# Optimization experiments

Hardware: AMD Instinct MI355X
Metric: run time of the kernel (lower is better)

The kernel has to match this reference:

```python
import jax, jax.numpy as jnp
import numpy as np

B, L, K, LI, D, NU, NI, C = 4096, 50, 10, 20, 64, 100000, 50000, 10


def _forward(users, items, u_items, u_items_mask, u_frids, u_frids_mask,
             u_frids_items, F_i, user_emb, item_emb, i_class,
             W1, b1, Wih, Whh, bih, bhh, W2, b2, W3, b3, W4, b4, W5, b5,
             W6, b6, alpha, lambdas):
    Bsz = users.shape[0]
    k = u_frids.shape[1]
    u = user_emb[users]                      # [B,d]
    i_e = item_emb[items]                    # [B,d]
    v = user_emb[u_frids]                    # [B,k,d]

    # ju_all = l1(cat(item_emb, i_class))
    ju_all = jnp.concatenate([item_emb, i_class], axis=1) @ W1 + b1   # [NI+1,d]
    ju = ju_all[u_items]                     # [B,L,d]

    # single-layer batch_first LSTM (torch gate order i,f,g,o)
    def step(carry, x):
        h, c = carry
        g = x @ Wih + h @ Whh + bih + bhh    # [B,4d]
        gi, gf, gg, go = jnp.split(g, 4, axis=1)
        c = jax.nn.sigmoid(gf) * c + jax.nn.sigmoid(gi) * jnp.tanh(gg)
        h = jax.nn.sigmoid(go) * jnp.tanh(c)
        return (h, c), h

    h0 = jnp.zeros((Bsz, ju.shape[-1]), ju.dtype)
    (_, _), hs = jax.lax.scan(step, (h0, h0), ju.transpose(1, 0, 2))
    out = hs.transpose(1, 0, 2)              # [B,L,d]
    hu = out[jnp.arange(Bsz), u_items_mask - 1]   # [B,d] last valid step

    hui = jnp.concatenate([hu, i_e, hu * i_e], axis=1) @ W2 + b2

    jv_all = jnp.concatenate([item_emb, i_class], axis=1) @ W3 + b3
    jv = jv_all[u_frids_items]               # [B,k,Li,d]
    # faithful to source: sum over item dim divided by friend count
    pv = jv.sum(axis=2) / u_frids_mask[:, None, None].astype(jv.dtype)  # [B,k,d]

    u_rep = jnp.broadcast_to(u[:, None, :], v.shape)
    at = jax.nn.leaky_relu(
        (jnp.concatenate([u_rep, v], axis=2) @ W4 + b4)[..., 0])  # [B,k]
    fmask = jnp.arange(k)[None, :] < u_frids_mask[:, None]
    auv = jnp.where(fmask,
                    jax.nn.softmax(jnp.where(fmask, at, -jnp.inf), axis=1),
                    0.0)                      # ragged softmax, zero-padded
    su = (pv * auv[:, :, None]).sum(axis=1)  # [B,d]
    sui = jnp.concatenate([su, i_e, su * i_e], axis=1) @ W5 + b5

    Fi1 = item_emb[F_i[:, 0, :]]             # [B,k,d]
    Fi2 = item_emb[F_i[:, 1, :]]
    i_rep = jnp.broadcast_to(i_e[:, None, :], Fi1.shape)
    s1 = jax.nn.leaky_relu(
        (jnp.concatenate([i_rep, Fi1], axis=2) @ W6 + b6)[..., 0])
    s2 = jax.nn.leaky_relu(
        (jnp.concatenate([i_rep, Fi2], axis=2) @ W6 + b6)[..., 0])
    # faithful to source: softmax over batch dim (dim=0)
    b1s = jax.nn.softmax(s1, axis=0)[:, :, None]
    b2s = jax.nn.softmax(s2, axis=0)[:, :, None]
    yi = alpha * (b1s * Fi1).sum(axis=1) + (1.0 - alpha) * (Fi2 * b2s).sum(axis=1)

    S = (lambdas[0] * (hu * yi).sum(1) + lambdas[1] * (hui * yi).sum(1)
         + lambdas[2] * (su * yi).sum(1) + lambdas[3] * (sui * yi).sum(1))
    return jax.nn.sigmoid(S)                 # rui [B]


def setup_inputs() -> dict:
    key = jax.random.key(0)
    ks = jax.random.split(key, 32)
    f32 = jnp.float32
    sd = 1.0 / np.sqrt(D)

    def lin(k, fan_in, fan_out):
        return sd * jax.random.normal(k, (fan_in, fan_out), dtype=f32)

    inp = {
        "users": jax.random.randint(ks[0], (B,), 0, NU),
        "items": jax.random.randint(ks[1], (B,), 0, NI),
        "u_items": jax.random.randint(ks[2], (B, L), 0, NI + 1),
        "u_items_mask": jax.random.randint(ks[3], (B,), 1, L + 1),
        "u_frids": jax.random.randint(ks[4], (B, K), 0, NU + 1),
        "u_frids_mask": jax.random.randint(ks[5], (B,), 1, K + 1),
        "u_frids_items": jax.random.randint(ks[6], (B, K, LI), 0, NI + 1),
        "F_i": jax.random.randint(ks[7], (B, 2, K), 0, NI + 1),
        "user_emb": sd * jax.random.normal(ks[8], (NU + 1, D), dtype=f32),
        "item_emb": sd * jax.random.normal(ks[9], (NI + 1, D), dtype=f32),
        "i_class": jax.nn.one_hot(
            jax.random.randint(ks[10], (NI + 1,), 0, C), C, dtype=f32),
        "W1": lin(ks[11], D + C, D), "b1": jnp.zeros((D,), f32),
        "Wih": lin(ks[12], D, 4 * D), "Whh": lin(ks[13], D, 4 * D),
        "bih": jnp.zeros((4 * D,), f32), "bhh": jnp.zeros((4 * D,), f32),
        "W2": lin(ks[14], 3 * D, D), "b2": jnp.zeros((D,), f32),
        "W3": lin(ks[15], D + C, D), "b3": jnp.zeros((D,), f32),
        "W4": lin(ks[16], 2 * D, 1), "b4": jnp.zeros((1,), f32),
        "W5": lin(ks[17], 3 * D, D), "b5": jnp.zeros((D,), f32),
        "W6": lin(ks[18], 2 * D, 1), "b6": jnp.zeros((1,), f32),
        "alpha": jnp.array([0.5], f32),
        "lambdas": jnp.array([0.5, 0.5, 0.5, 0.5], f32),
    }
    return inp


def reference(users, items, u_items, u_items_mask, u_frids, u_frids_mask,
              u_frids_items, F_i, user_emb, item_emb, i_class,
              W1, b1, Wih, Whh, bih, bhh, W2, b2, W3, b3, W4, b4, W5, b5,
              W6, b6, alpha, lambdas):
    return _forward(users, items, u_items, u_items_mask, u_frids,
                    u_frids_mask, u_frids_items, F_i, user_emb, item_emb,
                    i_class, W1, b1, Wih, Whh, bih, bhh, W2, b2, W3, b3,
                    W4, b4, W5, b5, W6, b6, alpha, lambdas)
```

## Files before the change

### kernel.cpp

```cpp
#include <hip/hip_runtime.h>

#define BSZ   4096
#define LSEQ  50
#define KFR   10
#define LI    20
#define DIM   64
#define NITEM 50001
#define CCLS  10

typedef __attribute__((ext_vector_type(8))) short short8;
typedef __attribute__((ext_vector_type(4))) float floatx4;

#define LOG2E 1.442695040888963f

__device__ inline unsigned short f2bf(float f) {
  unsigned u = __builtin_bit_cast(unsigned, f);
  u += 0x7FFF + ((u >> 16) & 1);
  return (unsigned short)(u >> 16);
}
__device__ inline float bf2f(unsigned short u) {
  return __builtin_bit_cast(float, ((unsigned)u) << 16);
}
__device__ inline float fast_exp(float x) {
  return __builtin_amdgcn_exp2f(x * LOG2E);
}
__device__ inline float fast_sigmoid(float x) {
  float e = __builtin_amdgcn_exp2f(-LOG2E * x);
  return __builtin_amdgcn_rcpf(1.0f + e);
}
__device__ inline float fast_tanh(float x) {
  float e = __builtin_amdgcn_exp2f(2.0f * LOG2E * x);
  return 1.0f - 2.0f * __builtin_amdgcn_rcpf(e + 1.0f);
}

__device__ __forceinline__ void item_block(int bid, int nblk,
                                 const float* __restrict__ item_emb,
                                 const float* __restrict__ i_class,
                                 const float* __restrict__ W1, const float* __restrict__ b1,
                                 const float* __restrict__ W3, const float* __restrict__ b3,
                                 unsigned short* __restrict__ ju_all,
                                 unsigned short* __restrict__ jv_all) {
  __shared__ float wcls[2][CCLS][64];
  for (int i = threadIdx.x; i < CCLS * 64; i += 256) {
    wcls[0][i >> 6][i & 63] = W1[(64 + (i >> 6)) * 64 + (i & 63)];
    wcls[1][i >> 6][i & 63] = W3[(64 + (i >> 6)) * 64 + (i & 63)];
  }
  __syncthreads();
  const int lane = threadIdx.x & 63;
  const int am = lane & 15, aq = lane >> 4;

  short8 bf[2][4][2];
  #pragma unroll
  for (int t = 0; t < 4; t++) {
    #pragma unroll
    for (int f = 0; f < 2; f++) {
      short8 v1, v3;
      #pragma unroll
      for (int j = 0; j < 8; j++) {
        int k = f * 32 + aq * 8 + j;
        int n = t * 16 + am;
        v1[j] = (short)f2bf(W1[k * 64 + n]);
        v3[j] = (short)f2bf(W3[k * 64 + n]);
      }
      bf[0][t][f] = v1; bf[1][t][f] = v3;
    }
  }
  float bias1[4], bias3[4];
  #pragma unroll
  for (int t = 0; t < 4; t++) { bias1[t] = b1[t * 16 + am]; bias3[t] = b3[t * 16 + am]; }

  const int gw = (bid * 256 + threadIdx.x) >> 6;
  const int nw = nblk * 4;
  const int ntiles = (NITEM + 15) / 16;
  for (int tile = gw; tile < ntiles; tile += nw) {
    const int r0 = tile * 16;
    const int row_a = r0 + am;
    const bool va = row_a < NITEM;
    short8 af[2];
    #pragma unroll
    for (int f = 0; f < 2; f++) {
      short8 v = {0, 0, 0, 0, 0, 0, 0, 0};
      if (va) {
        const float* p = item_emb + row_a * 64 + f * 32 + aq * 8;
        #pragma unroll
        for (int j = 0; j < 8; j++) v[j] = (short)f2bf(p[j]);
      }
      af[f] = v;
    }
    float cf = 0.f;
    if (va) {
      #pragma unroll
      for (int j = 1; j < CCLS; j++) cf += i_class[row_a * CCLS + j] * (float)j;
    }
    int ci_l = (int)(cf + 0.5f);

    floatx4 acc[2][4];
    #pragma unroll
    for (int mt = 0; mt < 2; mt++)
      #pragma unroll
      for (int t = 0; t < 4; t++) {
        floatx4 a = {0.f, 0.f, 0.f, 0.f};
        a = __builtin_amdgcn_mfma_f32_16x16x32_bf16(af[0], bf[mt][t][0], a, 0, 0, 0);
        a = __builtin_amdgcn_mfma_f32_16x16x32_bf16(af[1], bf[mt][t][1], a, 0, 0, 0);
        acc[mt][t] = a;
      }
    #pragma unroll
    for (int r = 0; r < 4; r++) {
      int row = aq * 4 + r;
      int grow = r0 + row;
      int ci = __shfl(ci_l, row, 64);
      if (grow < NITEM) {
        #pragma unroll
        for (int t = 0; t < 4; t++) {
          int n = t * 16 + am;
          ju_all[grow * 64 + n] = f2bf(acc[0][t][r] + wcls[0][ci][n] + bias1[t]);
          jv_all[grow * 64 + n] = f2bf(acc[1][t][r] + wcls[1][ci][n] + bias3[t]);
        }
      }
    }
  }
}

__device__ __forceinline__ void social_dots_block(int bid,
                         const int* __restrict__ users, const int* __restrict__ u_frids,
                         const int* __restrict__ u_frids_mask,
                         const float* __restrict__ user_emb,
                         const float* __restrict__ W4, const float* __restrict__ b4,
                         const int* __restrict__ items, const float* __restrict__ item_emb,
                         const int* __restrict__ F_i, const float* __restrict__ W6,
                         const float* __restrict__ b6,
                         float* __restrict__ auv, float* __restrict__ s12T) {
  const int b = (bid * 256 + threadIdx.x) >> 6;
  if (b >= BSZ) return;
  const int lane = threadIdx.x & 63;

  float w4a = W4[lane], w4b = W4[64 + lane];
  float w6a = W6[lane], w6b = W6[64 + lane];
  float p[32];
  p[0] = user_emb[users[b] * 64 + lane] * w4a;
  p[1] = item_emb[items[b] * 64 + lane] * w6a;
  #pragma unroll
  for (int k = 0; k < KFR; k++)
    p[2 + k] = user_emb[u_frids[b * KFR + k] * 64 + lane] * w4b;
  #pragma unroll
  for (int k = 0; k < KFR; k++) {
    p[12 + k] = item_emb[F_i[b * 2 * KFR + k] * 64 + lane] * w6b;
    p[22 + k] = item_emb[F_i[b * 2 * KFR + KFR + k] * 64 + lane] * w6b;
  }
  #pragma unroll
  for (int off = 1; off < 64; off <<= 1) {
    #pragma unroll
    for (int i = 0; i < 32; i++) p[i] += __shfl_xor(p[i], off, 64);
  }

  float du = p[0] + b4[0];
  float di = p[1] + b6[0];
  int km = u_frids_mask[b];
  float at[KFR];
  float M = -1e30f;
  #pragma unroll
  for (int k = 0; k < KFR; k++) {
    float s = p[2 + k] + du;
    at[k] = (s > 0.f) ? s : 0.01f * s;
    if (k < km) M = fmaxf(M, at[k]);
  }
  float E = 0.f;
  #pragma unroll
  for (int k = 0; k < KFR; k++) {
    at[k] = (k < km) ? fast_exp(at[k] - M) : 0.f;
    E += at[k];
  }
  float scale = __builtin_amdgcn_rcpf(E) * __builtin_amdgcn_rcpf((float)km);
  if (lane == 0) {
    #pragma unroll
    for (int k = 0; k < KFR; k++) {
      auv[b * KFR + k] = at[k] * scale;
      float r1 = p[12 + k] + di; r1 = (r1 > 0.f) ? r1 : 0.01f * r1;
      float r2 = p[22 + k] + di; r2 = (r2 > 0.f) ? r2 : 0.01f * r2;
      s12T[k * BSZ + b] = r1;
      s12T[(KFR + k) * BSZ + b] = r2;
    }
  }
}

__launch_bounds__(256, 1)
__global__ void k_item_dots(const float* __restrict__ item_emb,
                            const float* __restrict__ i_class,
                            const float* __restrict__ W1, const float* __restrict__ b1,
                            const float* __restrict__ W3, const float* __restrict__ b3,
                            unsigned short* __restrict__ ju_all,
                            unsigned short* __restrict__ jv_all,
                            const int* __restrict__ users, const int* __restrict__ u_frids,
                            const int* __restrict__ u_frids_mask,
                            const float* __restrict__ user_emb,
                            const float* __restrict__ W4, const float* __restrict__ b4,
                            const int* __restrict__ items,
                            const int* __restrict__ F_i, const float* __restrict__ W6,
                            const float* __restrict__ b6,
                            float* __restrict__ auv, float* __restrict__ s12T) {
  if (blockIdx.x < 512) {
    item_block(blockIdx.x, 512, item_emb, i_class, W1, b1, W3, b3, ju_all, jv_all);
  } else {
    social_dots_block(blockIdx.x - 512, users, u_frids, u_frids_mask, user_emb, W4, b4,
                      items, item_emb, F_i, W6, b6, auv, s12T);
  }
}

__device__ __forceinline__ void lstm_block(int bid,
                       const unsigned short* __restrict__ ju_all,
                       const int* __restrict__ u_items,
                       const int* __restrict__ u_items_mask,
                       const float* __restrict__ Wih, const float* __restrict__ Whh,
                       const float* __restrict__ bih, const float* __restrict__ bhh,
                       float* __restrict__ hu) {
  __shared__ __attribute__((aligned(16))) unsigned short xh[2][16 * 128];
  __shared__ int uidx[16][LSEQ];

  const int tid = threadIdx.x;
  const int lane = tid & 63;
  const int w = tid >> 6;
  const int b0 = bid * 16;
  const int am = lane & 15;
  const int aq = lane >> 4;
  const int dcol = w * 16 + am;

  short8 bfrag[4][4];
  #pragma unroll
  for (int g = 0; g < 4; g++) {
    const int ncol = g * 64 + dcol;
    #pragma unroll
    for (int f = 0; f < 4; f++) {
      short8 vv;
      #pragma unroll
      for (int j = 0; j < 8; j++) {
        int k = f * 32 + aq * 8 + j;
        float wv = (k < 64) ? Wih[k * 256 + ncol]
                            : Whh[(k - 64) * 256 + ncol];
        vv[j] = (short)f2bf(wv);
      }
      bfrag[g][f] = vv;
    }
  }
  for (int idx = tid; idx < 16 * LSEQ; idx += 256) {
    int m = idx / LSEQ, l = idx % LSEQ;
    uidx[m][l] = u_items[(b0 + m) * LSEQ + l];
  }
  __syncthreads();

  float bs[4];
  #pragma unroll
  for (int g = 0; g < 4; g++) bs[g] = bih[g * 64 + dcol] + bhh[g * 64 + dcol];
  float cst[4] = {0.f, 0.f, 0.f, 0.f};
  int maskr[4];
  #pragma unroll
  for (int r = 0; r < 4; r++) maskr[r] = u_items_mask[b0 + aq * 4 + r];

  {
    const int j = lane;
    #pragma unroll
    for (int i = 0; i < 4; i++) {
      int m = w + i * 4;
      xh[0][m * 128 + (((j >> 3) ^ m) << 3) + (j & 7)] = ju_all[uidx[m][0] * 64 + j];
      int k = 64 + j;
      xh[0][m * 128 + (((k >> 3) ^ m) << 3) + (k & 7)] = 0;
    }
  }
  __syncthreads();

  #pragma unroll 1
  for (int l = 0; l < LSEQ; l++) {
    const int p = l & 1, q = 1 - p;
    unsigned short xw[4];
    if (l < LSEQ - 1) {
      #pragma unroll
      for (int i = 0; i < 4; i++)
        xw[i] = ju_all[uidx[w + i * 4][l + 1] * 64 + lane];
    }
    short8 af[4];
    #pragma unroll
    for (int f = 0; f < 4; f++) {
      int chunk = (4 * f + aq) ^ am;
      af[f] = *(const short8*)&xh[p][am * 128 + chunk * 8];
    }
    floatx4 acc[4];
    #pragma unroll
    for (int g = 0; g < 4; g++) {
      floatx4 a = {0.f, 0.f, 0.f, 0.f};
      #pragma unroll
      for (int f = 0; f < 4; f++)
        a = __builtin_amdgcn_mfma_f32_16x16x32_bf16(af[f], bfrag[g][f], a, 0, 0, 0);
      acc[g] = a;
    }
    const int kcol = 64 + dcol;
    #pragma unroll
    for (int r = 0; r < 4; r++) {
      float gi = acc[0][r] + bs[0];
      float gf = acc[1][r] + bs[1];
      float gg = acc[2][r] + bs[2];
      float go = acc[3][r] + bs[3];
      float c = fast_sigmoid(gf) * cst[r] + fast_sigmoid(gi) * fast_tanh(gg);
      cst[r] = c;
      float h = fast_sigmoid(go) * fast_tanh(c);
      int m = aq * 4 + r;
      if (l == maskr[r] - 1) hu[(b0 + m) * 64 + dcol] = h;
      xh[q][m * 128 + (((kcol >> 3) ^ m) << 3) + (kcol & 7)] = f2bf(h);
    }
    if (l < LSEQ - 1) {
      const int j = lane;
      #pragma unroll
      for (int i = 0; i < 4; i++) {
        int m = w + i * 4;
        xh[q][m * 128 + (((j >> 3) ^ m) << 3) + (j & 7)] = xw[i];
      }
    }
    __syncthreads();
  }
}

__device__ __forceinline__ void social_pv_block(int bid,
                         const int* __restrict__ u_frids_items,
                         const unsigned short* __restrict__ jv_all,
                         const float* __restrict__ auv,
                         float* __restrict__ su) {
  const int b = (bid * 256 + threadIdx.x) >> 6;
  if (b >= BSZ) return;
  const int lane = threadIdx.x & 63;

  const int* fit = u_frids_items + b * (KFR * LI);
  int idx0 = fit[lane];
  int idx1 = fit[64 + lane];
  int idx2 = fit[128 + lane];
  int idx3 = (lane < 8) ? fit[192 + lane] : 0;

  float s = 0.f;
  #pragma unroll
  for (int k = 0; k < KFR; k++) {
    float a = auv[b * KFR + k];
    float pk = 0.f;
    #pragma unroll
    for (int li = 0; li < LI; li++) {
      int j = k * LI + li;
      int idx;
      if (j < 64)       idx = __shfl(idx0, j, 64);
      else if (j < 128) idx = __shfl(idx1, j - 64, 64);
      else if (j < 192) idx = __shfl(idx2, j - 128, 64);
      else              idx = __shfl(idx3, j - 192, 64);
      pk += bf2f(jv_all[idx * 64 + lane]);
    }
    s = fmaf(a, pk, s);
  }
  su[b * 64 + lane] = s;
}

__device__ __forceinline__ void colstats_block(int c,
                         const float* __restrict__ s12T, float* __restrict__ stats) {
  __shared__ float red[256];
  const float* col = s12T + c * BSZ;
  float m = -1e30f;
  for (int b = threadIdx.x; b < BSZ; b += 256) m = fmaxf(m, col[b]);
  red[threadIdx.x] = m;
  __syncthreads();
  for (int s = 128; s > 0; s >>= 1) {
    if (threadIdx.x < s) red[threadIdx.x] = fmaxf(red[threadIdx.x], red[threadIdx.x + s]);
    __syncthreads();
  }
  float M = red[0];
  __syncthreads();
  float e = 0.f;
  for (int b = threadIdx.x; b < BSZ; b += 256) e += fast_exp(col[b] - M);
  red[threadIdx.x] = e;
  __syncthreads();
  for (int s = 128; s > 0; s >>= 1) {
    if (threadIdx.x < s) red[threadIdx.x] += red[threadIdx.x + s];
    __syncthreads();
  }
  if (threadIdx.x == 0) { stats[c] = M; stats[20 + c] = red[0]; }
}

__launch_bounds__(256, 1)
__global__ void k_lstm_pv(const unsigned short* __restrict__ ju_all,
                          const int* __restrict__ u_items,
                          const int* __restrict__ u_items_mask,
                          const float* __restrict__ Wih, const float* __restrict__ Whh,
                          const float* __restrict__ bih, const float* __restrict__ bhh,
                          float* __restrict__ hu,
                          const int* __restrict__ u_frids_items,
                          const unsigned short* __restrict__ jv_all,
                          const float* __restrict__ auv, float* __restrict__ su,
                          const float* __restrict__ s12T, float* __restrict__ stats) {
  if (blockIdx.x < 256) {
    lstm_block(blockIdx.x, ju_all, u_items, u_items_mask, Wih, Whh, bih, bhh, hu);
  } else if (blockIdx.x < 1280) {
    social_pv_block(blockIdx.x - 256, u_frids_items, jv_all, auv, su);
  } else {
    colstats_block(blockIdx.x - 1280, s12T, stats);
  }
}

__launch_bounds__(512, 1)
__global__ void k_fuse_final(const float* __restrict__ hu, const float* __restrict__ su,
                             const int* __restrict__ items,
                             const float* __restrict__ item_emb,
                             const float* __restrict__ W2, const float* __restrict__ b2,
                             const float* __restrict__ W5, const float* __restrict__ b5,
                             const int* __restrict__ F_i,
                             const float* __restrict__ s12T, const float* __restrict__ stats,
                             const float* __restrict__ alpha, const float* __restrict__ lambdas,
                             float* __restrict__ out) {
  __shared__ float huis[16][66];
  __shared__ float suis[16][66];

  const int lane = threadIdx.x & 63;
  const int w = threadIdx.x >> 6;
  const int r0 = blockIdx.x * 16;

  const float al = alpha[0];
  const float l0 = lambdas[0], l1 = lambdas[1], l2 = lambdas[2], l3 = lambdas[3];

  float yi_r[4];
  float tp_r[4];

  if (w < 4) {
    const int mat = w >> 1;
    const int half = w & 1;
    const int am = lane & 15, aq = lane >> 4;

    const float* W = mat ? W5 : W2;
    const float* bb = mat ? b5 : b2;
    const float* xsrc = mat ? su : hu;

    short8 bfr[6][2];
    #pragma unroll
    for (int f = 0; f < 6; f++) {
      #pragma unroll
      for (int t = 0; t < 2; t++) {
        const int n = half * 32 + t * 16 + am;
        short8 v;
        #pragma unroll
        for (int j = 0; j < 8; j++) {
          int k = f * 32 + aq * 8 + j;
          v[j] = (short)f2bf(W[k * 64 + n]);
        }
        bfr[f][t] = v;
      }
    }
    float bias[2];
    #pragma unroll
    for (int t = 0; t < 2; t++) bias[t] = bb[half * 32 + t * 16 + am];

    const int row_a = r0 + am;
    const int it = items[row_a];
    short8 af[6];
    #pragma unroll
    for (int c = 0; c < 2; c++) {
      short8 vx, ve, vp;
      const float* xp = xsrc + row_a * 64 + c * 32 + aq * 8;
      const float* ep = item_emb + it * 64 + c * 32 + aq * 8;
      #pragma unroll
      for (int j = 0; j < 8; j++) {
        float x = xp[j], e = ep[j];
        vx[j] = (short)f2bf(x);
        ve[j] = (short)f2bf(e);
        vp[j] = (short)f2bf(x * e);
      }
      af[c] = vx; af[2 + c] = ve; af[4 + c] = vp;
    }
    floatx4 acc[2];
    #pragma unroll
    for (int t = 0; t < 2; t++) {
      floatx4 a = {0.f, 0.f, 0.f, 0.f};
      #pragma unroll
      for (int f = 0; f < 6; f++)
        a = __builtin_amdgcn_mfma_f32_16x16x32_bf16(af[f], bfr[f][t], a, 0, 0, 0);
      acc[t] = a;
    }
    float (*dst)[66] = mat ? suis : huis;
    #pragma unroll
    for (int t = 0; t < 2; t++)
      #pragma unroll
      for (int r = 0; r < 4; r++)
        dst[aq * 4 + r][half * 32 + t * 16 + am] = acc[t][r] + bias[t];
  } else {
    #pragma unroll
    for (int rr = 0; rr < 4; rr++) {
      const int r = r0 + (w - 4) * 4 + rr;
      float p1 = 0.f, p2 = 0.f;
      if (lane < KFR) {
        float v1 = s12T[lane * BSZ + r];
        float v2 = s12T[(KFR + lane) * BSZ + r];
        p1 = fast_exp(v1 - stats[lane]) * __builtin_amdgcn_rcpf(stats[20 + lane]);
        p2 = fast_exp(v2 - stats[KFR + lane]) * __builtin_amdgcn_rcpf(stats[30 + lane]);
      }
      float yi = 0.f;
      #pragma unroll
      for (int k = 0; k < KFR; k++) {
        float a1 = __shfl(p1, k, 64);
        float a2 = __shfl(p2, k, 64);
        int i1 = F_i[r * 2 * KFR + k];
        int i2 = F_i[r * 2 * KFR + KFR + k];
        yi += al * a1 * item_emb[i1 * 64 + lane] +
              (1.f - al) * a2 * item_emb[i2 * 64 + lane];
      }
      yi_r[rr] = yi;
      tp_r[rr] = l0 * hu[r * 64 + lane] + l2 * su[r * 64 + lane];
    }
  }
  __syncthreads();

  if (w >= 4) {
    #pragma unroll
    for (int rr = 0; rr < 4; rr++) {
      const int row = (w - 4) * 4 + rr;
      const int r = r0 + row;
      float t = tp_r[rr] + l1 * huis[row][lane] + l3 * suis[row][lane];
      float Sv = t * yi_r[rr];
      #pragma unroll
      for (int off = 1; off < 64; off <<= 1) Sv += __shfl_xor(Sv, off, 64);
      if (lane == 0) out[r] = fast_sigmoid(Sv);
    }
  }
}

extern "C" void kernel_launch(void* const* d_in, const int* in_sizes, int n_in,
                              void* d_out, int out_size, void* d_ws, size_t ws_size,
                              hipStream_t stream) {
  const int*   users        = (const int*)d_in[0];
  const int*   items        = (const int*)d_in[1];
  const int*   u_items      = (const int*)d_in[2];
  const int*   u_items_mask = (const int*)d_in[3];
  const int*   u_frids      = (const int*)d_in[4];
  const int*   u_frids_mask = (const int*)d_in[5];
  const int*   u_frids_items= (const int*)d_in[6];
  const int*   F_i          = (const int*)d_in[7];
  const float* user_emb     = (const float*)d_in[8];
  const float* item_emb     = (const float*)d_in[9];
  const float* i_class      = (const float*)d_in[10];
  const float* W1  = (const float*)d_in[11]; const float* b1  = (const float*)d_in[12];
  const float* Wih = (const float*)d_in[13]; const float* Whh = (const float*)d_in[14];
  const float* bih = (const float*)d_in[15]; const float* bhh = (const float*)d_in[16];
  const float* W2  = (const float*)d_in[17]; const float* b2  = (const float*)d_in[18];
  const float* W3  = (const float*)d_in[19]; const float* b3  = (const float*)d_in[20];
  const float* W4  = (const float*)d_in[21]; const float* b4  = (const float*)d_in[22];
  const float* W5  = (const float*)d_in[23]; const float* b5  = (const float*)d_in[24];
  const float* W6  = (const float*)d_in[25]; const float* b6  = (const float*)d_in[26];
  const float* alpha   = (const float*)d_in[27];
  const float* lambdas = (const float*)d_in[28];
  float* out = (float*)d_out;

  char* ws = (char*)d_ws;
  unsigned short* ju_all = (unsigned short*)(ws + 0);
  unsigned short* jv_all = (unsigned short*)(ws + 6400512);
  float* hu     = (float*)(ws + 12801024);
  float* su     = (float*)(ws + 13849600);
  float* s12T   = (float*)(ws + 14898176);
  float* stats  = (float*)(ws + 15225856);
  float* auv    = (float*)(ws + 15226112);

  k_item_dots<<<1536, 256, 0, stream>>>(item_emb, i_class, W1, b1, W3, b3, ju_all, jv_all,
                                        users, u_frids, u_frids_mask, user_emb, W4, b4,
                                        items, F_i, W6, b6, auv, s12T);
  k_lstm_pv<<<1300, 256, 0, stream>>>(ju_all, u_items, u_items_mask, Wih, Whh, bih, bhh, hu,
                                      u_frids_items, jv_all, auv, su, s12T, stats);
  k_fuse_final<<<256, 512, 0, stream>>>(hu, su, items, item_emb, W2, b2, W5, b5,
                                        F_i, s12T, stats, alpha, lambdas, out);
}
```

Measured before the change: 204.5 us.

## Split LSTM gate computation across two wave groups with LDS gate exchange

Each LSTM block grows from 4 to 8 waves. Each half of the block computes two of the four gate MFMAs and swaps the partial gate values through shared memory, so each wave runs half as many MFMAs per timestep on the serial recurrence. The social and colstats blocks are resized to 512 threads to match. In exchange, every timestep gets an extra __syncthreads and LDS round trip, and the block size doubles.

```diff
diff --git a/kernel.cpp b/kernel.cpp
--- a/kernel.cpp
+++ b/kernel.cpp
@@ -214,20 +214,23 @@
                        const float* __restrict__ bih, const float* __restrict__ bhh,
                        float* __restrict__ hu) {
   __shared__ __attribute__((aligned(16))) unsigned short xh[2][16 * 128];
+  __shared__ float exch[4][16][66];
   __shared__ int uidx[16][LSEQ];
 
   const int tid = threadIdx.x;
   const int lane = tid & 63;
   const int w = tid >> 6;
+  const int wg = w & 3;
+  const int gp = w >> 2;
   const int b0 = bid * 16;
   const int am = lane & 15;
   const int aq = lane >> 4;
-  const int dcol = w * 16 + am;
-
-  short8 bfrag[4][4];
-  #pragma unroll
-  for (int g = 0; g < 4; g++) {
-    const int ncol = g * 64 + dcol;
+  const int dcol = wg * 16 + am;
+
+  short8 bfrag[2][4];
+  #pragma unroll
+  for (int gg = 0; gg < 2; gg++) {
+    const int ncol = (2 * gp + gg) * 64 + dcol;
     #pragma unroll
     for (int f = 0; f < 4; f++) {
       short8 vv;
@@ -238,28 +241,29 @@
                             : Whh[(k - 64) * 256 + ncol];
         vv[j] = (short)f2bf(wv);
       }
-      bfrag[g][f] = vv;
-    }
-  }
-  for (int idx = tid; idx < 16 * LSEQ; idx += 256) {
+      bfrag[gg][f] = vv;
+    }
+  }
+  for (int idx = tid; idx < 16 * LSEQ; idx += 512) {
     int m = idx / LSEQ, l = idx % LSEQ;
     uidx[m][l] = u_items[(b0 + m) * LSEQ + l];
   }
   __syncthreads();
 
-  float bs[4];
-  #pragma unroll
-  for (int g = 0; g < 4; g++) bs[g] = bih[g * 64 + dcol] + bhh[g * 64 + dcol];
-  float cst[4] = {0.f, 0.f, 0.f, 0.f};
-  int maskr[4];
-  #pragma unroll
-  for (int r = 0; r < 4; r++) maskr[r] = u_items_mask[b0 + aq * 4 + r];
+  float bs[2];
+  #pragma unroll
+  for (int gg = 0; gg < 2; gg++)
+    bs[gg] = bih[(2 * gp + gg) * 64 + dcol] + bhh[(2 * gp + gg) * 64 + dcol];
+  float cst[2] = {0.f, 0.f};
+  int maskr[2];
+  #pragma unroll
+  for (int rr = 0; rr < 2; rr++) maskr[rr] = u_items_mask[b0 + aq * 4 + 2 * gp + rr];
 
   {
     const int j = lane;
     #pragma unroll
-    for (int i = 0; i < 4; i++) {
-      int m = w + i * 4;
+    for (int i = 0; i < 2; i++) {
+      int m = w * 2 + i;
       xh[0][m * 128 + (((j >> 3) ^ m) << 3) + (j & 7)] = ju_all[uidx[m][0] * 64 + j];
       int k = 64 + j;
       xh[0][m * 128 + (((k >> 3) ^ m) << 3) + (k & 7)] = 0;
@@ -270,11 +274,11 @@
   #pragma unroll 1
   for (int l = 0; l < LSEQ; l++) {
     const int p = l & 1, q = 1 - p;
-    unsigned short xw[4];
+    unsigned short xw[2];
     if (l < LSEQ - 1) {
       #pragma unroll
-      for (int i = 0; i < 4; i++)
-        xw[i] = ju_all[uidx[w + i * 4][l + 1] * 64 + lane];
+      for (int i = 0; i < 2; i++)
+        xw[i] = ju_all[uidx[w * 2 + i][l + 1] * 64 + lane];
     }
     short8 af[4];
     #pragma unroll
@@ -282,34 +286,49 @@
       int chunk = (4 * f + aq) ^ am;
       af[f] = *(const short8*)&xh[p][am * 128 + chunk * 8];
     }
-    floatx4 acc[4];
-    #pragma unroll
-    for (int g = 0; g < 4; g++) {
+    floatx4 acc[2];
+    #pragma unroll
+    for (int gg = 0; gg < 2; gg++) {
       floatx4 a = {0.f, 0.f, 0.f, 0.f};
       #pragma unroll
       for (int f = 0; f < 4; f++)
-        a = __builtin_amdgcn_mfma_f32_16x16x32_bf16(af[f], bfrag[g][f], a, 0, 0, 0);
-      acc[g] = a;
-    }
-    const int kcol = 64 + dcol;
-    #pragma unroll
-    for (int r = 0; r < 4; r++) {
-      float gi = acc[0][r] + bs[0];
-      float gf = acc[1][r] + bs[1];
-      float gg = acc[2][r] + bs[2];
-      float go = acc[3][r] + bs[3];
-      float c = fast_sigmoid(gf) * cst[r] + fast_sigmoid(gi) * fast_tanh(gg);
-      cst[r] = c;
+        a = __builtin_amdgcn_mfma_f32_16x16x32_bf16(af[f], bfrag[gg][f], a, 0, 0, 0);
+      acc[gg] = a;
+    }
+    #pragma unroll
+    for (int gg = 0; gg < 2; gg++) {
+      int gate = 2 * gp + gg;
+      #pragma unroll
+      for (int rr = 0; rr < 2; rr++) {
+        int r = 2 * (1 - gp) + rr;
+        exch[gate][aq * 4 + r][dcol] = acc[gg][r] + bs[gg];
+      }
+    }
+    __syncthreads();
+    #pragma unroll
+    for (int rr = 0; rr < 2; rr++) {
+      int r = 2 * gp + rr;
+      int m = aq * 4 + r;
+      float lo0 = acc[0][r] + bs[0];
+      float lo1 = acc[1][r] + bs[1];
+      float re0 = exch[2 * (1 - gp)][m][dcol];
+      float re1 = exch[2 * (1 - gp) + 1][m][dcol];
+      float gi  = gp ? re0 : lo0;
+      float gf  = gp ? re1 : lo1;
+      float gg_ = gp ? lo0 : re0;
+      float go  = gp ? lo1 : re1;
+      float c = fast_sigmoid(gf) * cst[rr] + fast_sigmoid(gi) * fast_tanh(gg_);
+      cst[rr] = c;
       float h = fast_sigmoid(go) * fast_tanh(c);
-      int m = aq * 4 + r;
-      if (l == maskr[r] - 1) hu[(b0 + m) * 64 + dcol] = h;
+      if (l == maskr[rr] - 1) hu[(b0 + m) * 64 + dcol] = h;
+      int kcol = 64 + dcol;
       xh[q][m * 128 + (((kcol >> 3) ^ m) << 3) + (kcol & 7)] = f2bf(h);
     }
     if (l < LSEQ - 1) {
       const int j = lane;
       #pragma unroll
-      for (int i = 0; i < 4; i++) {
-        int m = w + i * 4;
+      for (int i = 0; i < 2; i++) {
+        int m = w * 2 + i;
         xh[q][m * 128 + (((j >> 3) ^ m) << 3) + (j & 7)] = xw[i];
       }
     }
@@ -322,7 +341,7 @@
                          const unsigned short* __restrict__ jv_all,
                          const float* __restrict__ auv,
                          float* __restrict__ su) {
-  const int b = (bid * 256 + threadIdx.x) >> 6;
+  const int b = (bid * 512 + threadIdx.x) >> 6;
   if (b >= BSZ) return;
   const int lane = threadIdx.x & 63;
 
@@ -354,30 +373,30 @@
 
 __device__ __forceinline__ void colstats_block(int c,
                          const float* __restrict__ s12T, float* __restrict__ stats) {
-  __shared__ float red[256];
+  __shared__ float red[512];
   const float* col = s12T + c * BSZ;
   float m = -1e30f;
-  for (int b = threadIdx.x; b < BSZ; b += 256) m = fmaxf(m, col[b]);
+  for (int b = threadIdx.x; b < BSZ; b += 512) m = fmaxf(m, col[b]);
   red[threadIdx.x] = m;
   __syncthreads();
-  for (int s = 128; s > 0; s >>= 1) {
+  for (int s = 256; s > 0; s >>= 1) {
     if (threadIdx.x < s) red[threadIdx.x] = fmaxf(red[threadIdx.x], red[threadIdx.x + s]);
     __syncthreads();
   }
   float M = red[0];
   __syncthreads();
   float e = 0.f;
-  for (int b = threadIdx.x; b < BSZ; b += 256) e += fast_exp(col[b] - M);
+  for (int b = threadIdx.x; b < BSZ; b += 512) e += fast_exp(col[b] - M);
   red[threadIdx.x] = e;
   __syncthreads();
-  for (int s = 128; s > 0; s >>= 1) {
+  for (int s = 256; s > 0; s >>= 1) {
     if (threadIdx.x < s) red[threadIdx.x] += red[threadIdx.x + s];
     __syncthreads();
   }
   if (threadIdx.x == 0) { stats[c] = M; stats[20 + c] = red[0]; }
 }
 
-__launch_bounds__(256, 1)
+__launch_bounds__(512, 1)
 __global__ void k_lstm_pv(const unsigned short* __restrict__ ju_all,
                           const int* __restrict__ u_items,
                           const int* __restrict__ u_items_mask,
@@ -390,10 +409,10 @@
                           const float* __restrict__ s12T, float* __restrict__ stats) {
   if (blockIdx.x < 256) {
     lstm_block(blockIdx.x, ju_all, u_items, u_items_mask, Wih, Whh, bih, bhh, hu);
-  } else if (blockIdx.x < 1280) {
+  } else if (blockIdx.x < 768) {
     social_pv_block(blockIdx.x - 256, u_frids_items, jv_all, auv, su);
   } else {
-    colstats_block(blockIdx.x - 1280, s12T, stats);
+    colstats_block(blockIdx.x - 768, s12T, stats);
   }
 }
 
@@ -559,8 +578,8 @@
   k_item_dots<<<1536, 256, 0, stream>>>(item_emb, i_class, W1, b1, W3, b3, ju_all, jv_all,
                                         users, u_frids, u_frids_mask, user_emb, W4, b4,
                                         items, F_i, W6, b6, auv, s12T);
-  k_lstm_pv<<<1300, 256, 0, stream>>>(ju_all, u_items, u_items_mask, Wih, Whh, bih, bhh, hu,
-                                      u_frids_items, jv_all, auv, su, s12T, stats);
+  k_lstm_pv<<<788, 512, 0, stream>>>(ju_all, u_items, u_items_mask, Wih, Whh, bih, bhh, hu,
+                                     u_frids_items, jv_all, auv, su, s12T, stats);
   k_fuse_final<<<256, 512, 0, stream>>>(hu, su, items, item_emb, W2, b2, W5, b5,
                                         F_i, s12T, stats, alpha, lambdas, out);
 }
```

Result: slower. 220.2 us (+7.6%).

## Interleave social pv gather into LSTM blocks using extra producer warps

Applied to the files above, without the earlier changes.

Each LSTM block grows from 256 to 512 threads. Four warps keep running the serial LSTM recurrence, while four new warps spread the social pv gather (friend-item embedding sums weighted by attention) across the 50 timesteps, four users per warp. This removes the 1024 separate pv blocks and hides the gather latency behind the LSTM's per-step barrier stalls. Colstats blocks are widened to 512 threads to match. In exchange, pv work is tied to LSTM pacing and shares each step's syncthreads, and the pv warps load indices directly instead of broadcasting them with shuffles.

```diff
diff --git a/kernel.cpp b/kernel.cpp
--- a/kernel.cpp
+++ b/kernel.cpp
@@ -206,13 +206,17 @@
   }
 }
 
-__device__ __forceinline__ void lstm_block(int bid,
+__device__ __forceinline__ void lstm_pv_block(int bid,
                        const unsigned short* __restrict__ ju_all,
                        const int* __restrict__ u_items,
                        const int* __restrict__ u_items_mask,
                        const float* __restrict__ Wih, const float* __restrict__ Whh,
                        const float* __restrict__ bih, const float* __restrict__ bhh,
-                       float* __restrict__ hu) {
+                       float* __restrict__ hu,
+                       const int* __restrict__ u_frids_items,
+                       const unsigned short* __restrict__ jv_all,
+                       const float* __restrict__ auv,
+                       float* __restrict__ su) {
   __shared__ __attribute__((aligned(16))) unsigned short xh[2][16 * 128];
   __shared__ int uidx[16][LSEQ];
 
@@ -222,162 +226,157 @@
   const int b0 = bid * 16;
   const int am = lane & 15;
   const int aq = lane >> 4;
-  const int dcol = w * 16 + am;
+  const int dcol = (w & 3) * 16 + am;
 
   short8 bfrag[4][4];
-  #pragma unroll
-  for (int g = 0; g < 4; g++) {
-    const int ncol = g * 64 + dcol;
-    #pragma unroll
-    for (int f = 0; f < 4; f++) {
-      short8 vv;
-      #pragma unroll
-      for (int j = 0; j < 8; j++) {
-        int k = f * 32 + aq * 8 + j;
-        float wv = (k < 64) ? Wih[k * 256 + ncol]
-                            : Whh[(k - 64) * 256 + ncol];
-        vv[j] = (short)f2bf(wv);
-      }
-      bfrag[g][f] = vv;
-    }
-  }
-  for (int idx = tid; idx < 16 * LSEQ; idx += 256) {
-    int m = idx / LSEQ, l = idx % LSEQ;
-    uidx[m][l] = u_items[(b0 + m) * LSEQ + l];
-  }
-  __syncthreads();
-
   float bs[4];
-  #pragma unroll
-  for (int g = 0; g < 4; g++) bs[g] = bih[g * 64 + dcol] + bhh[g * 64 + dcol];
   float cst[4] = {0.f, 0.f, 0.f, 0.f};
   int maskr[4];
-  #pragma unroll
-  for (int r = 0; r < 4; r++) maskr[r] = u_items_mask[b0 + aq * 4 + r];
-
-  {
+  float pvs[4] = {0.f, 0.f, 0.f, 0.f};
+  const int pw = w - 4;
+
+  if (w < 4) {
+    #pragma unroll
+    for (int g = 0; g < 4; g++) {
+      const int ncol = g * 64 + dcol;
+      #pragma unroll
+      for (int f = 0; f < 4; f++) {
+        short8 vv;
+        #pragma unroll
+        for (int j = 0; j < 8; j++) {
+          int k = f * 32 + aq * 8 + j;
+          float wv = (k < 64) ? Wih[k * 256 + ncol]
+                              : Whh[(k - 64) * 256 + ncol];
+          vv[j] = (short)f2bf(wv);
+        }
+        bfrag[g][f] = vv;
+      }
+    }
+    for (int idx = tid; idx < 16 * LSEQ; idx += 256) {
+      int m = idx / LSEQ, l = idx % LSEQ;
+      uidx[m][l] = u_items[(b0 + m) * LSEQ + l];
+    }
+    #pragma unroll
+    for (int g = 0; g < 4; g++) bs[g] = bih[g * 64 + dcol] + bhh[g * 64 + dcol];
+    #pragma unroll
+    for (int r = 0; r < 4; r++) maskr[r] = u_items_mask[b0 + aq * 4 + r];
+  }
+  __syncthreads();
+
+  if (w < 4) {
     const int j = lane;
     #pragma unroll
     for (int i = 0; i < 4; i++) {
       int m = w + i * 4;
       xh[0][m * 128 + (((j >> 3) ^ m) << 3) + (j & 7)] = ju_all[uidx[m][0] * 64 + j];
-      int k = 64 + j;
-      xh[0][m * 128 + (((k >> 3) ^ m) << 3) + (k & 7)] = 0;
+      int k2 = 64 + j;
+      xh[0][m * 128 + (((k2 >> 3) ^ m) << 3) + (k2 & 7)] = 0;
     }
   }
   __syncthreads();
 
   #pragma unroll 1
   for (int l = 0; l < LSEQ; l++) {
-    const int p = l & 1, q = 1 - p;
-    unsigned short xw[4];
-    if (l < LSEQ - 1) {
-      #pragma unroll
-      for (int i = 0; i < 4; i++)
-        xw[i] = ju_all[uidx[w + i * 4][l + 1] * 64 + lane];
-    }
-    short8 af[4];
-    #pragma unroll
-    for (int f = 0; f < 4; f++) {
-      int chunk = (4 * f + aq) ^ am;
-      af[f] = *(const short8*)&xh[p][am * 128 + chunk * 8];
-    }
-    floatx4 acc[4];
-    #pragma unroll
-    for (int g = 0; g < 4; g++) {
-      floatx4 a = {0.f, 0.f, 0.f, 0.f};
-      #pragma unroll
-      for (int f = 0; f < 4; f++)
-        a = __builtin_amdgcn_mfma_f32_16x16x32_bf16(af[f], bfrag[g][f], a, 0, 0, 0);
-      acc[g] = a;
-    }
-    const int kcol = 64 + dcol;
-    #pragma unroll
-    for (int r = 0; r < 4; r++) {
-      float gi = acc[0][r] + bs[0];
-      float gf = acc[1][r] + bs[1];
-      float gg = acc[2][r] + bs[2];
-      float go = acc[3][r] + bs[3];
-      float c = fast_sigmoid(gf) * cst[r] + fast_sigmoid(gi) * fast_tanh(gg);
-      cst[r] = c;
-      float h = fast_sigmoid(go) * fast_tanh(c);
-      int m = aq * 4 + r;
-      if (l == maskr[r] - 1) hu[(b0 + m) * 64 + dcol] = h;
-      xh[q][m * 128 + (((kcol >> 3) ^ m) << 3) + (kcol & 7)] = f2bf(h);
-    }
-    if (l < LSEQ - 1) {
-      const int j = lane;
-      #pragma unroll
-      for (int i = 0; i < 4; i++) {
-        int m = w + i * 4;
-        xh[q][m * 128 + (((j >> 3) ^ m) << 3) + (j & 7)] = xw[i];
+    if (w < 4) {
+      const int p = l & 1, q = 1 - p;
+      unsigned short xw[4];
+      if (l < LSEQ - 1) {
+        #pragma unroll
+        for (int i = 0; i < 4; i++)
+          xw[i] = ju_all[uidx[w + i * 4][l + 1] * 64 + lane];
+      }
+      short8 af[4];
+      #pragma unroll
+      for (int f = 0; f < 4; f++) {
+        int chunk = (4 * f + aq) ^ am;
+        af[f] = *(const short8*)&xh[p][am * 128 + chunk * 8];
+      }
+      floatx4 acc[4];
+      #pragma unroll
+      for (int g = 0; g < 4; g++) {
+        floatx4 a = {0.f, 0.f, 0.f, 0.f};
+        #pragma unroll
+        for (int f = 0; f < 4; f++)
+          a = __builtin_amdgcn_mfma_f32_16x16x32_bf16(af[f], bfrag[g][f], a, 0, 0, 0);
+        acc[g] = a;
+      }
+      const int kcol = 64 + dcol;
+      #pragma unroll
+      for (int r = 0; r < 4; r++) {
+        float gi = acc[0][r] + bs[0];
+        float gf = acc[1][r] + bs[1];
+        float gg = acc[2][r] + bs[2];
+        float go = acc[3][r] + bs[3];
+        float c = fast_sigmoid(gf) * cst[r] + fast_sigmoid(gi) * fast_tanh(gg);
+        cst[r] = c;
+        float h = fast_sigmoid(go) * fast_tanh(c);
+        int m = aq * 4 + r;
+        if (l == maskr[r] - 1) hu[(b0 + m) * 64 + dcol] = h;
+        xh[q][m * 128 + (((kcol >> 3) ^ m) << 3) + (kcol & 7)] = f2bf(h);
+      }
+      if (l < LSEQ - 1) {
+        const int j = lane;
+        #pragma unroll
+        for (int i = 0; i < 4; i++) {
+          int m = w + i * 4;
+          xh[q][m * 128 + (((j >> 3) ^ m) << 3) + (j & 7)] = xw[i];
+        }
+      }
+    } else {
+      const int k = l / 5;
+      const int li0 = (l % 5) * 4;
+      #pragma unroll
+      for (int bb = 0; bb < 4; bb++) {
+        const int b = b0 + pw * 4 + bb;
+        const float a = auv[b * KFR + k];
+        const int* fit = u_frids_items + b * (KFR * LI) + k * LI + li0;
+        float accp = 0.f;
+        #pragma unroll
+        for (int jj = 0; jj < 4; jj++) {
+          int idx = fit[jj];
+          accp += bf2f(jv_all[idx * 64 + lane]);
+        }
+        pvs[bb] = fmaf(a, accp, pvs[bb]);
       }
     }
     __syncthreads();
   }
-}
-
-__device__ __forceinline__ void social_pv_block(int bid,
-                         const int* __restrict__ u_frids_items,
-                         const unsigned short* __restrict__ jv_all,
-                         const float* __restrict__ auv,
-                         float* __restrict__ su) {
-  const int b = (bid * 256 + threadIdx.x) >> 6;
-  if (b >= BSZ) return;
-  const int lane = threadIdx.x & 63;
-
-  const int* fit = u_frids_items + b * (KFR * LI);
-  int idx0 = fit[lane];
-  int idx1 = fit[64 + lane];
-  int idx2 = fit[128 + lane];
-  int idx3 = (lane < 8) ? fit[192 + lane] : 0;
-
-  float s = 0.f;
-  #pragma unroll
-  for (int k = 0; k < KFR; k++) {
-    float a = auv[b * KFR + k];
-    float pk = 0.f;
-    #pragma unroll
-    for (int li = 0; li < LI; li++) {
-      int j = k * LI + li;
-      int idx;
-      if (j < 64)       idx = __shfl(idx0, j, 64);
-      else if (j < 128) idx = __shfl(idx1, j - 64, 64);
-      else if (j < 192) idx = __shfl(idx2, j - 128, 64);
-      else              idx = __shfl(idx3, j - 192, 64);
-      pk += bf2f(jv_all[idx * 64 + lane]);
-    }
-    s = fmaf(a, pk, s);
-  }
-  su[b * 64 + lane] = s;
+
+  if (w >= 4) {
+    #pragma unroll
+    for (int bb = 0; bb < 4; bb++) {
+      const int b = b0 + pw * 4 + bb;
+      su[b * 64 + lane] = pvs[bb];
+    }
+  }
 }
 
 __device__ __forceinline__ void colstats_block(int c,
                          const float* __restrict__ s12T, float* __restrict__ stats) {
-  __shared__ float red[256];
+  __shared__ float red[512];
   const float* col = s12T + c * BSZ;
   float m = -1e30f;
-  for (int b = threadIdx.x; b < BSZ; b += 256) m = fmaxf(m, col[b]);
+  for (int b = threadIdx.x; b < BSZ; b += 512) m = fmaxf(m, col[b]);
   red[threadIdx.x] = m;
   __syncthreads();
-  for (int s = 128; s > 0; s >>= 1) {
+  for (int s = 256; s > 0; s >>= 1) {
     if (threadIdx.x < s) red[threadIdx.x] = fmaxf(red[threadIdx.x], red[threadIdx.x + s]);
     __syncthreads();
   }
   float M = red[0];
   __syncthreads();
   float e = 0.f;
-  for (int b = threadIdx.x; b < BSZ; b += 256) e += fast_exp(col[b] - M);
+  for (int b = threadIdx.x; b < BSZ; b += 512) e += fast_exp(col[b] - M);
   red[threadIdx.x] = e;
   __syncthreads();
-  for (int s = 128; s > 0; s >>= 1) {
+  for (int s = 256; s > 0; s >>= 1) {
     if (threadIdx.x < s) red[threadIdx.x] += red[threadIdx.x + s];
     __syncthreads();
   }
   if (threadIdx.x == 0) { stats[c] = M; stats[20 + c] = red[0]; }
 }
 
-__launch_bounds__(256, 1)
+__launch_bounds__(512, 2)
 __global__ void k_lstm_pv(const unsigned short* __restrict__ ju_all,
                           const int* __restrict__ u_items,
                           const int* __restrict__ u_items_mask,
@@ -389,11 +388,10 @@
                           const float* __restrict__ auv, float* __restrict__ su,
                           const float* __restrict__ s12T, float* __restrict__ stats) {
   if (blockIdx.x < 256) {
-    lstm_block(blockIdx.x, ju_all, u_items, u_items_mask, Wih, Whh, bih, bhh, hu);
-  } else if (blockIdx.x < 1280) {
-    social_pv_block(blockIdx.x - 256, u_frids_items, jv_all, auv, su);
+    lstm_pv_block(blockIdx.x, ju_all, u_items, u_items_mask, Wih, Whh, bih, bhh, hu,
+                  u_frids_items, jv_all, auv, su);
   } else {
-    colstats_block(blockIdx.x - 1280, s12T, stats);
+    colstats_block(blockIdx.x - 256, s12T, stats);
   }
 }
 
@@ -559,8 +557,8 @@
   k_item_dots<<<1536, 256, 0, stream>>>(item_emb, i_class, W1, b1, W3, b3, ju_all, jv_all,
                                         users, u_frids, u_frids_mask, user_emb, W4, b4,
                                         items, F_i, W6, b6, auv, s12T);
-  k_lstm_pv<<<1300, 256, 0, stream>>>(ju_all, u_items, u_items_mask, Wih, Whh, bih, bhh, hu,
-                                      u_frids_items, jv_all, auv, su, s12T, stats);
+  k_lstm_pv<<<276, 512, 0, stream>>>(ju_all, u_items, u_items_mask, Wih, Whh, bih, bhh, hu,
+                                     u_frids_items, jv_all, auv, su, s12T, stats);
   k_fuse_final<<<256, 512, 0, stream>>>(hu, su, items, item_emb, W2, b2, W5, b5,
                                         F_i, s12T, stats, alpha, lambdas, out);
 }
```

Result: slower. 221.6 us (+8.3%).

## Precompute LSTM input projection per item table row and gather gates in recurrence

Applied to the files above, without the earlier changes.

Folds the LSTM input-to-gate projection (ju @ Wih + biases) into the item-table pass, writing a bf16 per-item 4D gate table. The recurrent loop then gathers the precomputed gates per step and runs only the h @ Whh MFMAs, halving the serial MFMA work. The item pass gets twice as many blocks and does extra MFMA work plus a roughly 25 MB gate-table write. Each LSTM step now gathers 256-wide rows instead of 64-wide ones, which adds memory traffic and rounds the input projection to bf16 before accumulation.

```diff
diff --git a/kernel.cpp b/kernel.cpp
--- a/kernel.cpp
+++ b/kernel.cpp
@@ -38,15 +38,26 @@
                                  const float* __restrict__ i_class,
                                  const float* __restrict__ W1, const float* __restrict__ b1,
                                  const float* __restrict__ W3, const float* __restrict__ b3,
+                                 const float* __restrict__ Wih,
+                                 const float* __restrict__ bih, const float* __restrict__ bhh,
                                  unsigned short* __restrict__ ju_all,
-                                 unsigned short* __restrict__ jv_all) {
+                                 unsigned short* __restrict__ jv_all,
+                                 unsigned short* __restrict__ gxi) {
   __shared__ float wcls[2][CCLS][64];
+  __shared__ unsigned short wihT[256 * 64];
+  __shared__ unsigned short jt[4][16 * 64];
+
   for (int i = threadIdx.x; i < CCLS * 64; i += 256) {
     wcls[0][i >> 6][i & 63] = W1[(64 + (i >> 6)) * 64 + (i & 63)];
     wcls[1][i >> 6][i & 63] = W3[(64 + (i >> 6)) * 64 + (i & 63)];
   }
+  for (int idx = threadIdx.x; idx < 64 * 256; idx += 256) {
+    int k = idx >> 8, n = idx & 255;
+    wihT[n * 64 + (((k >> 3) ^ (n & 7)) << 3) + (k & 7)] = f2bf(Wih[k * 256 + n]);
+  }
   __syncthreads();
   const int lane = threadIdx.x & 63;
+  const int w = threadIdx.x >> 6;
   const int am = lane & 15, aq = lane >> 4;
 
   short8 bf[2][4][2];
@@ -68,6 +79,12 @@
   float bias1[4], bias3[4];
   #pragma unroll
   for (int t = 0; t < 4; t++) { bias1[t] = b1[t * 16 + am]; bias3[t] = b3[t * 16 + am]; }
+  float bs2[16];
+  #pragma unroll
+  for (int t2 = 0; t2 < 16; t2++) {
+    int n = t2 * 16 + am;
+    bs2[t2] = bih[n] + bhh[n];
+  }
 
   const int gw = (bid * 256 + threadIdx.x) >> 6;
   const int nw = nblk * 4;
@@ -113,9 +130,42 @@
         #pragma unroll
         for (int t = 0; t < 4; t++) {
           int n = t * 16 + am;
-          ju_all[grow * 64 + n] = f2bf(acc[0][t][r] + wcls[0][ci][n] + bias1[t]);
+          unsigned short jb = f2bf(acc[0][t][r] + wcls[0][ci][n] + bias1[t]);
+          ju_all[grow * 64 + n] = jb;
           jv_all[grow * 64 + n] = f2bf(acc[1][t][r] + wcls[1][ci][n] + bias3[t]);
+          jt[w][row * 64 + (((n >> 3) ^ (row & 7)) << 3) + (n & 7)] = jb;
         }
+      } else {
+        #pragma unroll
+        for (int t = 0; t < 4; t++) {
+          int n = t * 16 + am;
+          jt[w][row * 64 + (((n >> 3) ^ (row & 7)) << 3) + (n & 7)] = 0;
+        }
+      }
+    }
+    short8 aj[2];
+    #pragma unroll
+    for (int f = 0; f < 2; f++) {
+      int chunk = (f * 4 + aq) ^ (am & 7);
+      aj[f] = *(const short8*)&jt[w][am * 64 + chunk * 8];
+    }
+    #pragma unroll
+    for (int t2 = 0; t2 < 16; t2++) {
+      const int n = t2 * 16 + am;
+      short8 bw[2];
+      #pragma unroll
+      for (int f = 0; f < 2; f++) {
+        int chunk = (f * 4 + aq) ^ (n & 7);
+        bw[f] = *(const short8*)&wihT[n * 64 + chunk * 8];
+      }
+      floatx4 a2 = {0.f, 0.f, 0.f, 0.f};
+      a2 = __builtin_amdgcn_mfma_f32_16x16x32_bf16(aj[0], bw[0], a2, 0, 0, 0);
+      a2 = __builtin_amdgcn_mfma_f32_16x16x32_bf16(aj[1], bw[1], a2, 0, 0, 0);
+      #pragma unroll
+      for (int r = 0; r < 4; r++) {
+        int grow = r0 + aq * 4 + r;
+        if (grow < NITEM)
+          gxi[(size_t)grow * 256 + n] = f2bf(a2[r] + bs2[t2]);
       }
     }
   }
@@ -188,8 +238,11 @@
                             const float* __restrict__ i_class,
                             const float* __restrict__ W1, const float* __restrict__ b1,
                             const float* __restrict__ W3, const float* __restrict__ b3,
+                            const float* __restrict__ Wih,
+                            const float* __restrict__ bih, const float* __restrict__ bhh,
                             unsigned short* __restrict__ ju_all,
                             unsigned short* __restrict__ jv_all,
+                            unsigned short* __restrict__ gxi,
                             const int* __restrict__ users, const int* __restrict__ u_frids,
                             const int* __restrict__ u_frids_mask,
                             const float* __restrict__ user_emb,
@@ -198,20 +251,20 @@
                             const int* __restrict__ F_i, const float* __restrict__ W6,
                             const float* __restrict__ b6,
                             float* __restrict__ auv, float* __restrict__ s12T) {
-  if (blockIdx.x < 512) {
-    item_block(blockIdx.x, 512, item_emb, i_class, W1, b1, W3, b3, ju_all, jv_all);
+  if (blockIdx.x < 1024) {
+    item_block(blockIdx.x, 1024, item_emb, i_class, W1, b1, W3, b3, Wih, bih, bhh,
+               ju_all, jv_all, gxi);
   } else {
-    social_dots_block(blockIdx.x - 512, users, u_frids, u_frids_mask, user_emb, W4, b4,
+    social_dots_block(blockIdx.x - 1024, users, u_frids, u_frids_mask, user_emb, W4, b4,
                       items, item_emb, F_i, W6, b6, auv, s12T);
   }
 }
 
 __device__ __forceinline__ void lstm_block(int bid,
-                       const unsigned short* __restrict__ ju_all,
+                       const unsigned short* __restrict__ gxi,
                        const int* __restrict__ u_items,
                        const int* __restrict__ u_items_mask,
-                       const float* __restrict__ Wih, const float* __restrict__ Whh,
-                       const float* __restrict__ bih, const float* __restrict__ bhh,
+                       const float* __restrict__ Whh,
                        float* __restrict__ hu) {
   __shared__ __attribute__((aligned(16))) unsigned short xh[2][16 * 128];
   __shared__ int uidx[16][LSEQ];
@@ -224,19 +277,17 @@
   const int aq = lane >> 4;
   const int dcol = w * 16 + am;
 
-  short8 bfrag[4][4];
+  short8 bfrag[4][2];
   #pragma unroll
   for (int g = 0; g < 4; g++) {
     const int ncol = g * 64 + dcol;
     #pragma unroll
-    for (int f = 0; f < 4; f++) {
+    for (int f = 0; f < 2; f++) {
       short8 vv;
       #pragma unroll
       for (int j = 0; j < 8; j++) {
-        int k = f * 32 + aq * 8 + j;
-        float wv = (k < 64) ? Wih[k * 256 + ncol]
-                            : Whh[(k - 64) * 256 + ncol];
-        vv[j] = (short)f2bf(wv);
+        int kh = f * 32 + aq * 8 + j;
+        vv[j] = (short)f2bf(Whh[kh * 256 + ncol]);
       }
       bfrag[g][f] = vv;
     }
@@ -247,9 +298,6 @@
   }
   __syncthreads();
 
-  float bs[4];
-  #pragma unroll
-  for (int g = 0; g < 4; g++) bs[g] = bih[g * 64 + dcol] + bhh[g * 64 + dcol];
   float cst[4] = {0.f, 0.f, 0.f, 0.f};
   int maskr[4];
   #pragma unroll
@@ -260,44 +308,54 @@
     #pragma unroll
     for (int i = 0; i < 4; i++) {
       int m = w + i * 4;
-      xh[0][m * 128 + (((j >> 3) ^ m) << 3) + (j & 7)] = ju_all[uidx[m][0] * 64 + j];
-      int k = 64 + j;
-      xh[0][m * 128 + (((k >> 3) ^ m) << 3) + (k & 7)] = 0;
-    }
+      int k2 = 64 + j;
+      xh[0][m * 128 + (((k2 >> 3) ^ m) << 3) + (k2 & 7)] = 0;
+    }
+  }
+  unsigned short gxc[4][4];
+  #pragma unroll
+  for (int r = 0; r < 4; r++) {
+    int m = aq * 4 + r;
+    const unsigned short* gp = gxi + (size_t)uidx[m][0] * 256;
+    #pragma unroll
+    for (int g = 0; g < 4; g++) gxc[g][r] = gp[g * 64 + dcol];
   }
   __syncthreads();
 
   #pragma unroll 1
   for (int l = 0; l < LSEQ; l++) {
     const int p = l & 1, q = 1 - p;
-    unsigned short xw[4];
+    unsigned short gxn[4][4];
     if (l < LSEQ - 1) {
       #pragma unroll
-      for (int i = 0; i < 4; i++)
-        xw[i] = ju_all[uidx[w + i * 4][l + 1] * 64 + lane];
-    }
-    short8 af[4];
-    #pragma unroll
-    for (int f = 0; f < 4; f++) {
-      int chunk = (4 * f + aq) ^ am;
+      for (int r = 0; r < 4; r++) {
+        int m = aq * 4 + r;
+        const unsigned short* gp = gxi + (size_t)uidx[m][l + 1] * 256;
+        #pragma unroll
+        for (int g = 0; g < 4; g++) gxn[g][r] = gp[g * 64 + dcol];
+      }
+    }
+    short8 af[2];
+    #pragma unroll
+    for (int f = 0; f < 2; f++) {
+      int chunk = (4 * (f + 2) + aq) ^ am;
       af[f] = *(const short8*)&xh[p][am * 128 + chunk * 8];
     }
     floatx4 acc[4];
     #pragma unroll
     for (int g = 0; g < 4; g++) {
-      floatx4 a = {0.f, 0.f, 0.f, 0.f};
-      #pragma unroll
-      for (int f = 0; f < 4; f++)
-        a = __builtin_amdgcn_mfma_f32_16x16x32_bf16(af[f], bfrag[g][f], a, 0, 0, 0);
+      floatx4 a = {bf2f(gxc[g][0]), bf2f(gxc[g][1]), bf2f(gxc[g][2]), bf2f(gxc[g][3])};
+      a = __builtin_amdgcn_mfma_f32_16x16x32_bf16(af[0], bfrag[g][0], a, 0, 0, 0);
+      a = __builtin_amdgcn_mfma_f32_16x16x32_bf16(af[1], bfrag[g][1], a, 0, 0, 0);
       acc[g] = a;
     }
     const int kcol = 64 + dcol;
     #pragma unroll
     for (int r = 0; r < 4; r++) {
-      float gi = acc[0][r] + bs[0];
-      float gf = acc[1][r] + bs[1];
-      float gg = acc[2][r] + bs[2];
-      float go = acc[3][r] + bs[3];
+      float gi = acc[0][r];
+      float gf = acc[1][r];
+      float gg = acc[2][r];
+      float go = acc[3][r];
       float c = fast_sigmoid(gf) * cst[r] + fast_sigmoid(gi) * fast_tanh(gg);
       cst[r] = c;
       float h = fast_sigmoid(go) * fast_tanh(c);
@@ -306,12 +364,10 @@
       xh[q][m * 128 + (((kcol >> 3) ^ m) << 3) + (kcol & 7)] = f2bf(h);
     }
     if (l < LSEQ - 1) {
-      const int j = lane;
-      #pragma unroll
-      for (int i = 0; i < 4; i++) {
-        int m = w + i * 4;
-        xh[q][m * 128 + (((j >> 3) ^ m) << 3) + (j & 7)] = xw[i];
-      }
+      #pragma unroll
+      for (int g = 0; g < 4; g++)
+        #pragma unroll
+        for (int r = 0; r < 4; r++) gxc[g][r] = gxn[g][r];
     }
     __syncthreads();
   }
@@ -378,18 +434,17 @@
 }
 
 __launch_bounds__(256, 1)
-__global__ void k_lstm_pv(const unsigned short* __restrict__ ju_all,
+__global__ void k_lstm_pv(const unsigned short* __restrict__ gxi,
                           const int* __restrict__ u_items,
                           const int* __restrict__ u_items_mask,
-                          const float* __restrict__ Wih, const float* __restrict__ Whh,
-                          const float* __restrict__ bih, const float* __restrict__ bhh,
+                          const float* __restrict__ Whh,
                           float* __restrict__ hu,
                           const int* __restrict__ u_frids_items,
                           const unsigned short* __restrict__ jv_all,
                           const float* __restrict__ auv, float* __restrict__ su,
                           const float* __restrict__ s12T, float* __restrict__ stats) {
   if (blockIdx.x < 256) {
-    lstm_block(blockIdx.x, ju_all, u_items, u_items_mask, Wih, Whh, bih, bhh, hu);
+    lstm_block(blockIdx.x, gxi, u_items, u_items_mask, Whh, hu);
   } else if (blockIdx.x < 1280) {
     social_pv_block(blockIdx.x - 256, u_frids_items, jv_all, auv, su);
   } else {
@@ -555,11 +610,13 @@
   float* s12T   = (float*)(ws + 14898176);
   float* stats  = (float*)(ws + 15225856);
   float* auv    = (float*)(ws + 15226112);
-
-  k_item_dots<<<1536, 256, 0, stream>>>(item_emb, i_class, W1, b1, W3, b3, ju_all, jv_all,
+  unsigned short* gxi = (unsigned short*)(ws + 15389952);
+
+  k_item_dots<<<2048, 256, 0, stream>>>(item_emb, i_class, W1, b1, W3, b3, Wih, bih, bhh,
+                                        ju_all, jv_all, gxi,
                                         users, u_frids, u_frids_mask, user_emb, W4, b4,
                                         items, F_i, W6, b6, auv, s12T);
-  k_lstm_pv<<<1300, 256, 0, stream>>>(ju_all, u_items, u_items_mask, Wih, Whh, bih, bhh, hu,
+  k_lstm_pv<<<1300, 256, 0, stream>>>(gxi, u_items, u_items_mask, Whh, hu,
                                       u_frids_items, jv_all, auv, su, s12T, stats);
   k_fuse_final<<<256, 512, 0, stream>>>(hu, su, items, item_emb, W2, b2, W5, b5,
                                         F_i, s12T, stats, alpha, lambdas, out);
```

Measured after the change: 236.8 us. +15.8%, slower.
